# Performance work log

Hardware: AMD Instinct MI355X
Metric: run time of the kernel (lower is better)

Reference implementation:

```python
import jax, jax.numpy as jnp
import numpy as np

N_NODES = 10000
N_EDGES = 160000
N_GRAPHS = 20
IN_F, HID, OUT_F, HEADS = 50, 256, 121, 4
NEG_SLOPE = 0.2
GN_EPS = 1e-5
SM_EPS = 1e-16


def _with_self_loops(edge_index, n):
    loop = jnp.arange(n, dtype=edge_index.dtype)
    src = jnp.concatenate([edge_index[0], loop])
    dst = jnp.concatenate([edge_index[1], loop])
    return src, dst


def gat_conv(x, W, att_src, att_dst, bias, src, dst, heads, out_c):
    # PyG GATConv: linear -> per-node attention halves -> edge leaky_relu
    # -> softmax over incoming edges of each dst -> weighted scatter-sum.
    n = x.shape[0]
    h = (x @ W).reshape(n, heads, out_c)                # [N,H,C]
    a_s = (h * att_src).sum(-1)                          # [N,H]
    a_d = (h * att_dst).sum(-1)                          # [N,H]
    e = a_s[src] + a_d[dst]                              # [E,H]
    e = jnp.where(e > 0, e, NEG_SLOPE * e)
    e_max = jax.ops.segment_max(e, dst, num_segments=n)  # self-loops cover all dst
    ex = jnp.exp(e - e_max[dst])
    den = jax.ops.segment_sum(ex, dst, num_segments=n)
    alpha = ex / (den[dst] + SM_EPS)                     # [E,H]
    out = jax.ops.segment_sum(h[src] * alpha[..., None], dst, num_segments=n)
    return out.reshape(n, heads * out_c) + bias


def graph_norm(x, batch, weight, bias, mean_scale, n_graphs):
    cnt = jax.ops.segment_sum(jnp.ones((x.shape[0],), x.dtype), batch,
                              num_segments=n_graphs)[:, None]    # [G,1]
    mean = jax.ops.segment_sum(x, batch, num_segments=n_graphs) / cnt
    ctr = x - mean[batch] * mean_scale
    var = jax.ops.segment_sum(ctr * ctr, batch, num_segments=n_graphs) / cnt
    inv = jax.lax.rsqrt(var + GN_EPS)
    return weight * ctr * inv[batch] + bias


def setup_inputs() -> dict:
    key = jax.random.key(0)
    ks = jax.random.split(key, 24)
    d = {}
    d['x'] = jax.random.normal(ks[0], (N_NODES, IN_F), jnp.float32)
    d['edge_index'] = jax.random.randint(ks[1], (2, N_EDGES), 0, N_NODES, jnp.int64 if jax.config.jax_enable_x64 else jnp.int32)
    d['batch'] = jnp.sort(jax.random.randint(ks[2], (N_NODES,), 0, N_GRAPHS))
    def glorot(k, shape):
        fan = shape[0] + shape[-1]
        return jax.random.normal(k, shape, jnp.float32) * np.sqrt(2.0 / fan)
    dims = [(IN_F, HEADS, HID), (HEADS * HID, HEADS, HID), (HEADS * HID, HEADS, HID), (HEADS * HID, 1, OUT_F)]
    i = 3
    for li, (fin, h, c) in enumerate(dims, 1):
        d[f'W{li}'] = glorot(ks[i], (fin, h * c)); i += 1
        d[f'as{li}'] = glorot(ks[i], (h, c)); i += 1
        d[f'ad{li}'] = glorot(ks[i], (h, c)); i += 1
        d[f'b{li}'] = jnp.zeros((h * c,), jnp.float32)
    for li in (1, 2, 3):
        w = HEADS * HID
        d[f'gw{li}'] = jnp.ones((w,), jnp.float32)
        d[f'gb{li}'] = jnp.zeros((w,), jnp.float32)
        d[f'ga{li}'] = jnp.ones((w,), jnp.float32)
    return d


def reference(x, edge_index, batch,
              W1, as1, ad1, b1, W2, as2, ad2, b2, W3, as3, ad3, b3, W4, as4, ad4, b4,
              gw1, gb1, ga1, gw2, gb2, ga2, gw3, gb3, ga3):
    src, dst = _with_self_loops(edge_index, N_NODES)
    h = gat_conv(x, W1, as1, ad1, b1, src, dst, HEADS, HID)
    h = jax.nn.elu(graph_norm(h, batch, gw1, gb1, ga1, N_GRAPHS))
    h = gat_conv(h, W2, as2, ad2, b2, src, dst, HEADS, HID)
    h = jax.nn.elu(graph_norm(h, batch, gw2, gb2, ga2, N_GRAPHS))
    h = gat_conv(h, W3, as3, ad3, b3, src, dst, HEADS, HID)
    h = jax.nn.elu(graph_norm(h, batch, gw3, gb3, ga3, N_GRAPHS))
    return gat_conv(h, W4, as4, ad4, b4, src, dst, 1, OUT_F)
```

## Files before the change

kernel.cpp:

```cpp
#include <hip/hip_runtime.h>
#include <math.h>

#define NN 10000
#define NE 160000
#define E2 (NE + NN)
#define NG 20
#define MPAD 10112

typedef __attribute__((ext_vector_type(8))) short short8;
typedef __attribute__((ext_vector_type(4))) float f32x4;

__device__ inline unsigned short f2bf(float f){
  unsigned u = __float_as_uint(f);
  unsigned r = u + 0x7FFFu + ((u >> 16) & 1u);
  return (unsigned short)(r >> 16);
}
__device__ inline float bf2f(unsigned short h){ return __uint_as_float(((unsigned)h) << 16); }

__device__ inline void gload_lds16(const void* g, void* l){
  __builtin_amdgcn_global_load_lds((const __attribute__((address_space(1))) void*)g,
                                   (__attribute__((address_space(3))) void*)l, 16, 0, 0);
}

__global__ void k_gptr(const int* __restrict__ batch, int* __restrict__ gptr){
  int g = threadIdx.x;
  if (g > NG) return;
  int lo = 0, hi = NN;
  while (lo < hi){ int mid = (lo+hi)>>1; if (batch[mid] < g) lo = mid+1; else hi = mid; }
  gptr[g] = lo;
}

__global__ void k_count(const int* __restrict__ ei, int* __restrict__ cnt){
  int e = blockIdx.x*256 + threadIdx.x;
  if (e >= E2) return;
  int d = (e < NE) ? ei[NE + e] : (e - NE);
  atomicAdd(&cnt[d], 1);
}

__global__ void k_scan(const int* __restrict__ cnt, int* __restrict__ ptr){
  __shared__ int tpre[256];
  __shared__ int tsum[256];
  int tid = threadIdx.x;
  const int per = (NN + 255)/256;
  int base = tid*per;
  int s = 0;
  for (int i=0;i<per;i++){ int idx=base+i; if (idx<NN) s += cnt[idx]; }
  tsum[tid] = s;
  __syncthreads();
  if (tid == 0){
    int run = 0;
    for (int i=0;i<256;i++){ tpre[i]=run; run += tsum[i]; }
    ptr[NN] = run;
  }
  __syncthreads();
  int run = tpre[tid];
  for (int i=0;i<per;i++){ int idx=base+i; if (idx<NN){ ptr[idx]=run; run += cnt[idx]; } }
}

__global__ void k_copy(const int* __restrict__ src, int* __restrict__ dst){
  int i = blockIdx.x*256 + threadIdx.x;
  if (i < NN) dst[i] = src[i];
}

__global__ void k_scatter(const int* __restrict__ ei, int* __restrict__ fill, int* __restrict__ csrc){
  int e = blockIdx.x*256 + threadIdx.x;
  if (e >= E2) return;
  int s, d;
  if (e < NE){ s = ei[e]; d = ei[NE + e]; } else { s = d = e - NE; }
  int pos = atomicAdd(&fill[d], 1);
  csrc[pos] = s;
}

__global__ void k_xconv(const float* __restrict__ x, unsigned short* __restrict__ xbf){
  int i = blockIdx.x*256 + threadIdx.x;
  if (i >= MPAD*64) return;
  int r = i >> 6, c = i & 63;
  float v = (r < NN && c < 50) ? x[r*50 + c] : 0.f;
  xbf[i] = f2bf(v);
}

__global__ void k_wconv(const float* __restrict__ W, unsigned short* __restrict__ Wt,
                        int K, int N, int Kpad, int Npad){
  int i = blockIdx.x*256 + threadIdx.x;
  if (i >= Npad*Kpad) return;
  int nn = i / Kpad, kk = i - nn*Kpad;
  float v = (nn < N && kk < K) ? W[(size_t)kk*N + nn] : 0.f;
  Wt[i] = f2bf(v);
}

template<int TBM, int TBN>
__global__ __launch_bounds__(256) void k_mfma_gemm(
    const unsigned short* __restrict__ A,
    const unsigned short* __restrict__ Bt,
    unsigned short* __restrict__ Cbf,
    int M, int K, int FS, int ncb)
{
  constexpr int MFR = TBM/32;
  constexpr int NFR = TBN/32;
  constexpr int ABYTES = TBM*64;
  constexpr int BBYTES = TBN*64;
  __shared__ unsigned short sA[2*TBM*32];
  __shared__ unsigned short sB[2*TBN*32];
  const int tid = threadIdx.x;
  const int wave = tid >> 6;
  const int lane = tid & 63;
  const int nwg = gridDim.x;
  const int q = nwg >> 3, rmod = nwg & 7;
  const int xcd = blockIdx.x & 7, idx = blockIdx.x >> 3;
  const int wg = (xcd < rmod) ? (xcd*(q+1) + idx) : (rmod*(q+1) + (xcd - rmod)*q + idx);
  const int rowt = wg / ncb;
  const int colt = wg - rowt*ncb;
  const int row0 = rowt * TBM;
  const int col0 = colt * TBN;
  const int wr = (wave >> 1) * (TBM/2);
  const int wc = (wave & 1) * (TBN/2);
  f32x4 acc[MFR][NFR];
  #pragma unroll
  for (int i=0;i<MFR;i++)
    #pragma unroll
    for (int j=0;j<NFR;j++){ acc[i][j][0]=0.f; acc[i][j][1]=0.f; acc[i][j][2]=0.f; acc[i][j][3]=0.f; }

  const int arow = tid >> 2;
  const int achn = (tid & 3) ^ ((arow >> 1) & 3);
  const unsigned short* aSrc = A + (size_t)(row0 + arow)*K + achn*8;
  const unsigned short* bSrc = Bt + (size_t)(col0 + arow)*K + achn*8;
  char* ldsA = (char*)sA + wave*1024;
  char* ldsB = (char*)sB + wave*1024;

  auto STAGE = [&](int k0, int buf){
    #pragma unroll
    for (int h=0; h<TBM/64; h++) gload_lds16(aSrc + (size_t)h*64*K + k0, ldsA + buf*ABYTES + h*4096);
    #pragma unroll
    for (int h=0; h<TBN/64; h++) gload_lds16(bSrc + (size_t)h*64*K + k0, ldsB + buf*BBYTES + h*4096);
  };

  const int NT = K >> 5;
  const int kch = lane >> 4;
  const int rlo = lane & 15;

  STAGE(0, 0);
  if (NT > 1) STAGE(32, 1);
  if constexpr (TBM+TBN == 256) asm volatile("s_waitcnt vmcnt(4)" ::: "memory");
  else                          asm volatile("s_waitcnt vmcnt(2)" ::: "memory");
  __builtin_amdgcn_sched_barrier(0);
  __builtin_amdgcn_s_barrier();

  int cur = 0;
  for (int t = 0; t < NT; ++t){
    const unsigned short* bA = sA + cur*(TBM*32);
    const unsigned short* bB = sB + cur*(TBN*32);
    short8 af[MFR], bfr[NFR];
    #pragma unroll
    for (int m=0;m<MFR;m++){
      int r = wr + m*16 + rlo;
      af[m] = *(const short8*)(bA + r*32 + ((kch ^ ((r>>1)&3))<<3));
    }
    #pragma unroll
    for (int n=0;n<NFR;n++){
      int r = wc + n*16 + rlo;
      bfr[n] = *(const short8*)(bB + r*32 + ((kch ^ ((r>>1)&3))<<3));
    }
    asm volatile("s_waitcnt lgkmcnt(0)" ::: "memory");
    __builtin_amdgcn_sched_barrier(0);
    __builtin_amdgcn_s_barrier();
    if (t+2 < NT) STAGE((t+2) << 5, cur);
    #pragma unroll
    for (int m=0;m<MFR;m++)
      #pragma unroll
      for (int n=0;n<NFR;n++)
        acc[m][n] = __builtin_amdgcn_mfma_f32_16x16x32_bf16(af[m], bfr[n], acc[m][n], 0, 0, 0);
    if (t+1 < NT){
      if (t+2 < NT){
        if constexpr (TBM+TBN == 256) asm volatile("s_waitcnt vmcnt(4)" ::: "memory");
        else                          asm volatile("s_waitcnt vmcnt(2)" ::: "memory");
      } else {
        asm volatile("s_waitcnt vmcnt(0)" ::: "memory");
      }
      __builtin_amdgcn_sched_barrier(0);
      __builtin_amdgcn_s_barrier();
    }
    cur ^= 1;
  }
  const int cr = (lane >> 4) * 4;
  const int cc = lane & 15;
  #pragma unroll
  for (int m=0;m<MFR;m++){
    #pragma unroll
    for (int n=0;n<NFR;n++){
      int col = col0 + wc + n*16 + cc;
      #pragma unroll
      for (int r=0;r<4;r++){
        int row = row0 + wr + m*16 + cr + r;
        if (row < M) Cbf[(size_t)row*FS + col] = f2bf(acc[m][n][r]);
      }
    }
  }
}

__global__ void k_attprep(const unsigned short* __restrict__ h, const float* __restrict__ atts,
                          const float* __restrict__ attd,
                          float* __restrict__ a_s, float* __restrict__ a_d, int H, int C, int FS){
  int node = blockIdx.x, head = blockIdx.y;
  int lane = threadIdx.x;
  const unsigned short* hp = h + (size_t)node*FS + head*C;
  const float* sp = atts + head*C;
  const float* dp = attd + head*C;
  float ss = 0.f, sd = 0.f;
  for (int c = lane; c < C; c += 64){ float v = bf2f(hp[c]); ss += v*sp[c]; sd += v*dp[c]; }
  #pragma unroll
  for (int o = 32; o; o >>= 1){ ss += __shfl_down(ss, o); sd += __shfl_down(sd, o); }
  if (lane == 0){ a_s[node*H + head] = ss; a_d[node*H + head] = sd; }
}

__global__ void k_alpha(const float* __restrict__ a_s, const float* __restrict__ a_d,
                        const int* __restrict__ ptr, const int* __restrict__ csrc,
                        float* __restrict__ alphaT, int H, int LH){
  int node = blockIdx.x;
  int lane = threadIdx.x;
  int beg = ptr[node], deg = ptr[node+1] - beg;
  int items = deg << LH;
  int hh = lane & (H-1);
  float ad = a_d[node*H + hh];
  float mx = -INFINITY;
  for (int i = lane; i < items; i += 64){
    int e = i >> LH;
    int s = csrc[beg + e];
    float ev = a_s[s*H + hh] + ad;
    ev = ev > 0.f ? ev : 0.2f*ev;
    mx = fmaxf(mx, ev);
  }
  for (int o = H; o < 64; o <<= 1) mx = fmaxf(mx, __shfl_xor(mx, o));
  float den = 0.f;
  for (int i = lane; i < items; i += 64){
    int e = i >> LH;
    int s = csrc[beg + e];
    float ev = a_s[s*H + hh] + ad;
    ev = ev > 0.f ? ev : 0.2f*ev;
    den += __expf(ev - mx);
  }
  for (int o = H; o < 64; o <<= 1) den += __shfl_xor(den, o);
  float inv = 1.f / (den + 1e-16f);
  for (int i = lane; i < items; i += 64){
    int e = i >> LH;
    int s = csrc[beg + e];
    float ev = a_s[s*H + hh] + ad;
    ev = ev > 0.f ? ev : 0.2f*ev;
    alphaT[(size_t)hh*E2 + beg + e] = __expf(ev - mx) * inv;
  }
}

template<int L>
__global__ __launch_bounds__(256) void k_gather2(
    const unsigned short* __restrict__ h, int FS,
    const float* __restrict__ alphaT,
    const int* __restrict__ ptr, const int* __restrict__ csrc,
    const float* __restrict__ bias, float* __restrict__ out,
    int F, int C, int outF)
{
  constexpr int NGRP = 256 / L;
  constexpr int CS = L * 8;
  const int node = blockIdx.x;
  const int head = blockIdx.y;
  const int colbase = head * C;
  const int beg = ptr[node], deg = ptr[node+1] - beg;
  __shared__ int ssrc[256];
  __shared__ float sal[256];
  __shared__ float red[NGRP * CS];
  const int tid = threadIdx.x;
  const int grp = tid / L, li = tid % L;
  const int c0 = colbase + li*8;
  const float* aT = alphaT + (size_t)head*E2 + beg;
  float acc[8] = {0.f,0.f,0.f,0.f,0.f,0.f,0.f,0.f};
  for (int b0 = 0; b0 < deg; b0 += 256){
    int bn = min(256, deg - b0);
    if (tid < bn){ ssrc[tid] = csrc[beg + b0 + tid]; sal[tid] = aT[b0 + tid]; }
    __syncthreads();
    for (int e = grp; e < bn; e += NGRP){
      int s = ssrc[e];
      float al = sal[e];
      short8 v = *(const short8*)(h + (size_t)s*FS + c0);
      #pragma unroll
      for (int j=0;j<8;j++) acc[j] += bf2f((unsigned short)v[j]) * al;
    }
    __syncthreads();
  }
  #pragma unroll
  for (int j=0;j<8;j++) red[grp*CS + li*8 + j] = acc[j];
  __syncthreads();
  for (int c = tid; c < CS; c += 256){
    float s = 0.f;
    #pragma unroll
    for (int g=0; g<NGRP; g++) s += red[g*CS + c];
    int oc = colbase + c;
    if (oc < F) out[(size_t)node*outF + oc] = s + bias[oc];
  }
}

#define NSPLIT 16
__global__ void k_gnstats(const float* __restrict__ x, const int* __restrict__ gptr,
                          float* __restrict__ gsum, float* __restrict__ gsq, int F){
  int g = blockIdx.x, cc = blockIdx.y, sp = blockIdx.z;
  int c = cc*256 + threadIdx.x;
  if (c >= F) return;
  int beg = gptr[g], end = gptr[g+1];
  int n = end - beg;
  int per = (n + NSPLIT - 1) / NSPLIT;
  int nb = beg + sp*per, ne = min(end, nb + per);
  if (ne <= nb) return;
  float s = 0.f, q = 0.f;
  for (int i = nb; i < ne; i++){ float v = x[(size_t)i*F + c]; s += v; q += v*v; }
  atomicAdd(&gsum[g*F + c], s);
  atomicAdd(&gsq[g*F + c], q);
}

__global__ void k_coef(const float* __restrict__ gsum, const float* __restrict__ gsq, const int* __restrict__ gptr,
                       const float* __restrict__ w, const float* __restrict__ b, const float* __restrict__ ms,
                       float* __restrict__ cA, float* __restrict__ cB, int F){
  int i = blockIdx.x*256 + threadIdx.x;
  if (i >= NG*F) return;
  int g = i / F, c = i - g*F;
  float cntf = (float)(gptr[g+1] - gptr[g]);
  float m = gsum[i] / cntf;
  float s = ms[c];
  float ex2 = gsq[i] / cntf;
  float var = ex2 - 2.f*s*m*m + s*s*m*m;
  float inv = rsqrtf(var + 1e-5f);
  float wa = w[c]*inv;
  cA[i] = wa;
  cB[i] = b[c] - wa*m*s;
}

__global__ void k_applyelu(const float* __restrict__ x, const int* __restrict__ batch,
                           const float* __restrict__ cA, const float* __restrict__ cB,
                           unsigned short* __restrict__ obf, int F){
  size_t i = (size_t)blockIdx.x*256 + threadIdx.x;
  if (i >= (size_t)NN*F) return;
  int node = (int)(i / F);
  int c = (int)(i - (size_t)node*F);
  int g = batch[node];
  float y = cA[g*F + c]*x[i] + cB[g*F + c];
  y = y > 0.f ? y : expm1f(y);
  obf[i] = f2bf(y);
}

extern "C" void kernel_launch(void* const* d_in, const int* in_sizes, int n_in,
                              void* d_out, int out_size, void* d_ws, size_t ws_size,
                              hipStream_t stream){
  (void)in_sizes; (void)n_in; (void)out_size; (void)ws_size;
  const float* x     = (const float*)d_in[0];
  const int*   ei    = (const int*)d_in[1];
  const int*   batch = (const int*)d_in[2];
  const float* W[4]  = {(const float*)d_in[3],  (const float*)d_in[7],  (const float*)d_in[11], (const float*)d_in[15]};
  const float* AS[4] = {(const float*)d_in[4],  (const float*)d_in[8],  (const float*)d_in[12], (const float*)d_in[16]};
  const float* AD[4] = {(const float*)d_in[5],  (const float*)d_in[9],  (const float*)d_in[13], (const float*)d_in[17]};
  const float* BI[4] = {(const float*)d_in[6],  (const float*)d_in[10], (const float*)d_in[14], (const float*)d_in[18]};
  const float* GW[3] = {(const float*)d_in[19], (const float*)d_in[22], (const float*)d_in[25]};
  const float* GB[3] = {(const float*)d_in[20], (const float*)d_in[23], (const float*)d_in[26]};
  const float* GA[3] = {(const float*)d_in[21], (const float*)d_in[24], (const float*)d_in[27]};

  float* ws   = (float*)d_ws;
  float* bufB = ws;
  float* a_s  = bufB + (size_t)NN*1024;
  float* a_d  = a_s + (size_t)NN*4;
  float* gsum = a_d + (size_t)NN*4;
  float* gsq  = gsum + (size_t)NG*1024;
  float* cA   = gsq  + (size_t)NG*1024;
  float* cB   = cA   + (size_t)NG*1024;
  float* alphaT = cB + (size_t)NG*1024;
  int* ptr  = (int*)(alphaT + (size_t)4*E2);
  int* fill = ptr + (NN + 8);
  int* csrc = fill + (NN + 8);
  int* gptr = csrc + E2;
  unsigned short* xbf = (unsigned short*)(gptr + 24);
  unsigned short* abf = xbf + (size_t)MPAD*64;
  unsigned short* hbf = abf + (size_t)MPAD*1024;
  unsigned short* Wt  = hbf + (size_t)NN*1024;

  hipMemsetAsync(fill, 0, sizeof(int)*(NN+1), stream);
  k_gptr<<<1, 32, 0, stream>>>(batch, gptr);
  k_count<<<(E2+255)/256, 256, 0, stream>>>(ei, fill);
  k_scan<<<1, 256, 0, stream>>>(fill, ptr);
  k_copy<<<(NN+255)/256, 256, 0, stream>>>(ptr, fill);
  k_scatter<<<(E2+255)/256, 256, 0, stream>>>(ei, fill, csrc);
  k_xconv<<<(MPAD*64+255)/256, 256, 0, stream>>>(x, xbf);

  const int Kp[4]  = {64, 1024, 1024, 1024};
  const int Kr[4]  = {50, 1024, 1024, 1024};
  const int Np[4]  = {1024, 1024, 1024, 128};
  for (int li = 0; li < 4; ++li){
    int H = (li == 3) ? 1 : 4;
    int LH = (li == 3) ? 0 : 2;
    int C = (li == 3) ? 121 : 256;
    int F = H*C;
    int FS = Np[li];
    const unsigned short* Ain = (li == 0) ? xbf : abf;
    k_wconv<<<(Np[li]*Kp[li]+255)/256, 256, 0, stream>>>(W[li], Wt, Kr[li], F, Kp[li], Np[li]);
    if (li < 3){
      int ncb = Np[li]/128;
      int nwg = (MPAD/128) * ncb;
      k_mfma_gemm<128,128><<<nwg, 256, 0, stream>>>(Ain, Wt, hbf, NN, Kp[li], FS, ncb);
    } else {
      int ncb = Np[li]/64;
      int nwg = (MPAD/64) * ncb;
      k_mfma_gemm<64,64><<<nwg, 256, 0, stream>>>(Ain, Wt, hbf, NN, Kp[li], FS, ncb);
    }
    k_attprep<<<dim3(NN, H), 64, 0, stream>>>(hbf, AS[li], AD[li], a_s, a_d, H, C, FS);
    k_alpha<<<NN, 64, 0, stream>>>(a_s, a_d, ptr, csrc, alphaT, H, LH);
    float* gout = (li == 3) ? (float*)d_out : bufB;
    if (li < 3)
      k_gather2<32><<<dim3(NN, 4), 256, 0, stream>>>(hbf, FS, alphaT, ptr, csrc, BI[li], gout, F, C, F);
    else
      k_gather2<16><<<dim3(NN, 1), 256, 0, stream>>>(hbf, FS, alphaT, ptr, csrc, BI[li], gout, F, C, F);
    if (li < 3){
      hipMemsetAsync(gsum, 0, sizeof(float)*2*NG*1024, stream);
      k_gnstats<<<dim3(NG, (F+255)/256, NSPLIT), 256, 0, stream>>>(bufB, gptr, gsum, gsq, F);
      k_coef<<<(NG*F + 255)/256, 256, 0, stream>>>(gsum, gsq, gptr, GW[li], GB[li], GA[li], cA, cB, F);
      size_t tot = (size_t)NN*F;
      k_applyelu<<<(unsigned)((tot + 255)/256), 256, 0, stream>>>(bufB, batch, cA, cB, abf, F);
    }
  }
}
```

Measured before the change: 550.7 us.

## Fuse softmax into wave-per-node gather and shrink GEMM tile for hidden layers

```diff
diff --git a/kernel.cpp b/kernel.cpp
--- a/kernel.cpp
+++ b/kernel.cpp
@@ -8,6 +8,7 @@
 #define MPAD 10112
 
 typedef __attribute__((ext_vector_type(8))) short short8;
+typedef __attribute__((ext_vector_type(4))) short short4v;
 typedef __attribute__((ext_vector_type(4))) float f32x4;
 
 __device__ inline unsigned short f2bf(float f){
@@ -99,6 +100,7 @@
   constexpr int NFR = TBN/32;
   constexpr int ABYTES = TBM*64;
   constexpr int BBYTES = TBN*64;
+  constexpr int LPS = TBM/64 + TBN/64;
   __shared__ unsigned short sA[2*TBM*32];
   __shared__ unsigned short sB[2*TBN*32];
   const int tid = threadIdx.x;
@@ -140,8 +142,9 @@
 
   STAGE(0, 0);
   if (NT > 1) STAGE(32, 1);
-  if constexpr (TBM+TBN == 256) asm volatile("s_waitcnt vmcnt(4)" ::: "memory");
-  else                          asm volatile("s_waitcnt vmcnt(2)" ::: "memory");
+  if constexpr (LPS==4)      asm volatile("s_waitcnt vmcnt(4)" ::: "memory");
+  else if constexpr (LPS==3) asm volatile("s_waitcnt vmcnt(3)" ::: "memory");
+  else                       asm volatile("s_waitcnt vmcnt(2)" ::: "memory");
   __builtin_amdgcn_sched_barrier(0);
   __builtin_amdgcn_s_barrier();
 
@@ -171,8 +174,9 @@
         acc[m][n] = __builtin_amdgcn_mfma_f32_16x16x32_bf16(af[m], bfr[n], acc[m][n], 0, 0, 0);
     if (t+1 < NT){
       if (t+2 < NT){
-        if constexpr (TBM+TBN == 256) asm volatile("s_waitcnt vmcnt(4)" ::: "memory");
-        else                          asm volatile("s_waitcnt vmcnt(2)" ::: "memory");
+        if constexpr (LPS==4)      asm volatile("s_waitcnt vmcnt(4)" ::: "memory");
+        else if constexpr (LPS==3) asm volatile("s_waitcnt vmcnt(3)" ::: "memory");
+        else                       asm volatile("s_waitcnt vmcnt(2)" ::: "memory");
       } else {
         asm volatile("s_waitcnt vmcnt(0)" ::: "memory");
       }
@@ -194,6 +198,32 @@
         if (row < M) Cbf[(size_t)row*FS + col] = f2bf(acc[m][n][r]);
       }
     }
+  }
+}
+
+__global__ __launch_bounds__(256) void k_attprepw(
+    const unsigned short* __restrict__ h,
+    const float* __restrict__ atts, const float* __restrict__ attd,
+    float* __restrict__ a_s, float* __restrict__ a_d)
+{
+  const int wid = threadIdx.x >> 6, lane = threadIdx.x & 63;
+  const int node = blockIdx.x*4 + wid;
+  const unsigned short* hp = h + (size_t)node*1024 + lane*16;
+  short8 v0 = *(const short8*)hp;
+  short8 v1 = *(const short8*)(hp+8);
+  const float* sp = atts + lane*16;
+  const float* dp = attd + lane*16;
+  float ss = 0.f, sd = 0.f;
+  #pragma unroll
+  for (int j=0;j<8;j++){ float f = bf2f((unsigned short)v0[j]); ss += f*sp[j];   sd += f*dp[j]; }
+  #pragma unroll
+  for (int j=0;j<8;j++){ float f = bf2f((unsigned short)v1[j]); ss += f*sp[8+j]; sd += f*dp[8+j]; }
+  #pragma unroll
+  for (int o=8;o;o>>=1){ ss += __shfl_xor(ss,o); sd += __shfl_xor(sd,o); }
+  if ((lane & 15) == 0){
+    int hh = lane >> 4;
+    a_s[node*4 + hh] = ss;
+    a_d[node*4 + hh] = sd;
   }
 }
 
@@ -249,6 +279,79 @@
   }
 }
 
+__global__ __launch_bounds__(256) void k_gatherw(
+    const unsigned short* __restrict__ h,
+    const float* __restrict__ a_s, const float* __restrict__ a_d,
+    const int* __restrict__ ptr, const int* __restrict__ csrc,
+    const float* __restrict__ bias, float* __restrict__ out)
+{
+  __shared__ float sal[4][64*4];
+  __shared__ int ssn[4][64];
+  const int wid = threadIdx.x >> 6, lane = threadIdx.x & 63;
+  const int node = blockIdx.x*4 + wid;
+  const int hh = lane >> 4;
+  const int beg = ptr[node], deg = ptr[node+1] - beg;
+  f32x4 ad4 = *(const f32x4*)(a_d + node*4);
+  float acc[16], acc2[16];
+  #pragma unroll
+  for (int j=0;j<16;j++){ acc[j]=0.f; acc2[j]=0.f; }
+  f32x4 denp = {0.f,0.f,0.f,0.f};
+  const unsigned short* hb = h + lane*16;
+
+  for (int c0 = 0; c0 < deg; c0 += 64){
+    int n = min(64, deg - c0);
+    if (lane < n){
+      int s = csrc[beg + c0 + lane];
+      f32x4 as4 = *(const f32x4*)(a_s + s*4);
+      f32x4 e4;
+      #pragma unroll
+      for (int k2=0;k2<4;k2++){
+        float ev = as4[k2] + ad4[k2];
+        ev = ev > 0.f ? ev : 0.2f*ev;
+        float x = __expf(ev);
+        e4[k2] = x;
+        denp[k2] += x;
+      }
+      *(f32x4*)&sal[wid][lane*4] = e4;
+      ssn[wid][lane] = s;
+    }
+    int e = 0;
+    for (; e + 1 < n; e += 2){
+      int sA_ = ssn[wid][e], sB_ = ssn[wid][e+1];
+      float aA = sal[wid][e*4 + hh], aB = sal[wid][(e+1)*4 + hh];
+      const unsigned short* pA = hb + (size_t)sA_*1024;
+      const unsigned short* pB = hb + (size_t)sB_*1024;
+      short8 uA0 = *(const short8*)pA, uA1 = *(const short8*)(pA+8);
+      short8 uB0 = *(const short8*)pB, uB1 = *(const short8*)(pB+8);
+      #pragma unroll
+      for (int j=0;j<8;j++){ acc[j]   += bf2f((unsigned short)uA0[j])*aA;
+                             acc[8+j] += bf2f((unsigned short)uA1[j])*aA; }
+      #pragma unroll
+      for (int j=0;j<8;j++){ acc2[j]   += bf2f((unsigned short)uB0[j])*aB;
+                             acc2[8+j] += bf2f((unsigned short)uB1[j])*aB; }
+    }
+    if (e < n){
+      int sA_ = ssn[wid][e];
+      float aA = sal[wid][e*4 + hh];
+      const unsigned short* pA = hb + (size_t)sA_*1024;
+      short8 uA0 = *(const short8*)pA, uA1 = *(const short8*)(pA+8);
+      #pragma unroll
+      for (int j=0;j<8;j++){ acc[j]   += bf2f((unsigned short)uA0[j])*aA;
+                             acc[8+j] += bf2f((unsigned short)uA1[j])*aA; }
+    }
+  }
+  #pragma unroll
+  for (int o=32;o;o>>=1){
+    #pragma unroll
+    for (int k2=0;k2<4;k2++) denp[k2] += __shfl_xor(denp[k2], o);
+  }
+  float inv = 1.f / (denp[hh] + 1e-16f);
+  float* op = out + (size_t)node*1024 + lane*16;
+  const float* bp = bias + lane*16;
+  #pragma unroll
+  for (int j=0;j<16;j++) op[j] = (acc[j]+acc2[j])*inv + bp[j];
+}
+
 template<int L>
 __global__ __launch_bounds__(256) void k_gather2(
     const unsigned short* __restrict__ h, int FS,
@@ -264,7 +367,7 @@
   const int colbase = head * C;
   const int beg = ptr[node], deg = ptr[node+1] - beg;
   __shared__ int ssrc[256];
-  __shared__ float sal[256];
+  __shared__ float salv[256];
   __shared__ float red[NGRP * CS];
   const int tid = threadIdx.x;
   const int grp = tid / L, li = tid % L;
@@ -273,11 +376,11 @@
   float acc[8] = {0.f,0.f,0.f,0.f,0.f,0.f,0.f,0.f};
   for (int b0 = 0; b0 < deg; b0 += 256){
     int bn = min(256, deg - b0);
-    if (tid < bn){ ssrc[tid] = csrc[beg + b0 + tid]; sal[tid] = aT[b0 + tid]; }
+    if (tid < bn){ ssrc[tid] = csrc[beg + b0 + tid]; salv[tid] = aT[b0 + tid]; }
     __syncthreads();
     for (int e = grp; e < bn; e += NGRP){
       int s = ssrc[e];
-      float al = sal[e];
+      float al = salv[e];
       short8 v = *(const short8*)(h + (size_t)s*FS + c0);
       #pragma unroll
       for (int j=0;j<8;j++) acc[j] += bf2f((unsigned short)v[j]) * al;
@@ -397,26 +500,22 @@
     k_wconv<<<(Np[li]*Kp[li]+255)/256, 256, 0, stream>>>(W[li], Wt, Kr[li], F, Kp[li], Np[li]);
     if (li < 3){
       int ncb = Np[li]/128;
-      int nwg = (MPAD/128) * ncb;
-      k_mfma_gemm<128,128><<<nwg, 256, 0, stream>>>(Ain, Wt, hbf, NN, Kp[li], FS, ncb);
-    } else {
-      int ncb = Np[li]/64;
       int nwg = (MPAD/64) * ncb;
-      k_mfma_gemm<64,64><<<nwg, 256, 0, stream>>>(Ain, Wt, hbf, NN, Kp[li], FS, ncb);
-    }
-    k_attprep<<<dim3(NN, H), 64, 0, stream>>>(hbf, AS[li], AD[li], a_s, a_d, H, C, FS);
-    k_alpha<<<NN, 64, 0, stream>>>(a_s, a_d, ptr, csrc, alphaT, H, LH);
-    float* gout = (li == 3) ? (float*)d_out : bufB;
-    if (li < 3)
-      k_gather2<32><<<dim3(NN, 4), 256, 0, stream>>>(hbf, FS, alphaT, ptr, csrc, BI[li], gout, F, C, F);
-    else
-      k_gather2<16><<<dim3(NN, 1), 256, 0, stream>>>(hbf, FS, alphaT, ptr, csrc, BI[li], gout, F, C, F);
-    if (li < 3){
+      k_mfma_gemm<64,128><<<nwg, 256, 0, stream>>>(Ain, Wt, hbf, NN, Kp[li], FS, ncb);
+      k_attprepw<<<NN/4, 256, 0, stream>>>(hbf, AS[li], AD[li], a_s, a_d);
+      k_gatherw<<<NN/4, 256, 0, stream>>>(hbf, a_s, a_d, ptr, csrc, BI[li], bufB);
       hipMemsetAsync(gsum, 0, sizeof(float)*2*NG*1024, stream);
       k_gnstats<<<dim3(NG, (F+255)/256, NSPLIT), 256, 0, stream>>>(bufB, gptr, gsum, gsq, F);
       k_coef<<<(NG*F + 255)/256, 256, 0, stream>>>(gsum, gsq, gptr, GW[li], GB[li], GA[li], cA, cB, F);
       size_t tot = (size_t)NN*F;
       k_applyelu<<<(unsigned)((tot + 255)/256), 256, 0, stream>>>(bufB, batch, cA, cB, abf, F);
-    }
-  }
-}
+    } else {
+      int ncb = Np[li]/64;
+      int nwg = (MPAD/64) * ncb;
+      k_mfma_gemm<64,64><<<nwg, 256, 0, stream>>>(Ain, Wt, hbf, NN, Kp[li], FS, ncb);
+      k_attprep<<<dim3(NN, 1), 64, 0, stream>>>(hbf, AS[li], AD[li], a_s, a_d, H, C, FS);
+      k_alpha<<<NN, 64, 0, stream>>>(a_s, a_d, ptr, csrc, alphaT, H, LH);
+      k_gather2<16><<<dim3(NN, 1), 256, 0, stream>>>(hbf, FS, alphaT, ptr, csrc, BI[li], (float*)d_out, F, C, F);
+    }
+  }
+}
```

Result: faster. 519.0 us (-5.8%).
